# Optimization experiments

Hardware: AMD Instinct MI355X
Metric: run time of the kernel (lower is better)

The kernel has to match this reference:

```python
import jax, jax.numpy as jnp
import numpy as np

B, T = 64, 1024
VOCAB, EMBED, HIDDEN = 55, 64, 128


def setup_inputs() -> dict:
    key = jax.random.key(0)
    ks = jax.random.split(key, 15)
    stdv = 1.0 / np.sqrt(HIDDEN)
    u = lambda k, s: jax.random.uniform(k, s, jnp.float32, -stdv, stdv)
    return {
        "x": jax.random.randint(ks[0], (B, T), 0, VOCAB),
        "emb": jax.random.normal(ks[1], (VOCAB, EMBED), jnp.float32),
        "w_ih0": u(ks[2], (HIDDEN, EMBED)),
        "b_ih0": u(ks[3], (HIDDEN,)),
        "w_hh0": u(ks[4], (HIDDEN, HIDDEN)),
        "b_hh0": u(ks[5], (HIDDEN,)),
        "w_ih1": u(ks[6], (HIDDEN, HIDDEN)),
        "b_ih1": u(ks[7], (HIDDEN,)),
        "w_hh1": u(ks[8], (HIDDEN, HIDDEN)),
        "b_hh1": u(ks[9], (HIDDEN,)),
        "attn_w": u(ks[10], (HIDDEN, HIDDEN)),
        "attn_b": u(ks[11], (HIDDEN,)),
        "fc_w": u(ks[12], (VOCAB, 2 * HIDDEN)),
        "fc_b": u(ks[13], (VOCAB,)),
    }


def reference(x, emb, w_ih0, b_ih0, w_hh0, b_hh0, w_ih1, b_ih1, w_hh1, b_hh1,
              attn_w, attn_b, fc_w, fc_b):
    Bx, Tx = x.shape
    H = w_hh0.shape[0]
    e = emb[x]  # [B, T, E]

    def step(carry, x_t):  # x_t: [B, E]
        h0, h1 = carry
        h0 = jnp.tanh(x_t @ w_ih0.T + b_ih0 + h0 @ w_hh0.T + b_hh0)
        h1 = jnp.tanh(h0 @ w_ih1.T + b_ih1 + h1 @ w_hh1.T + b_hh1)
        return (h0, h1), h1

    init = (jnp.zeros((Bx, H), e.dtype), jnp.zeros((Bx, H), e.dtype))
    _, outs = jax.lax.scan(step, init, jnp.swapaxes(e, 0, 1))  # [T, B, H]
    outs = jnp.swapaxes(outs, 0, 1)  # [B, T, H]

    Q = outs @ attn_w.T + attn_b  # [B, T, H]
    scores = jnp.einsum('bth,bsh->bts', Q, outs) / jnp.sqrt(jnp.asarray(H, e.dtype))
    causal = jnp.tril(jnp.ones((Tx, Tx), bool))  # [T, T]
    scores = jnp.where(causal[None], scores, jnp.asarray(-jnp.inf, scores.dtype))
    attn = jax.nn.softmax(scores, axis=-1)
    context = jnp.einsum('bts,bsh->bth', attn, outs)  # [B, T, H]

    combined = jnp.concatenate([outs, context], axis=-1)  # [B, T, 2H]
    logits = combined @ fc_w.T + fc_b  # [B, T, vocab]
    return logits
```

## Files before the change

kernel.cpp:

```cpp
#include <hip/hip_runtime.h>
#include <hip/hip_bf16.h>
#include <cstdint>
#include <cstddef>


typedef __attribute__((ext_vector_type(8))) short short8;
typedef __attribute__((ext_vector_type(4))) float f32x4;

__device__ __forceinline__ float bf2f(unsigned short u) {
    union { unsigned int i; float f; } c; c.i = ((unsigned int)u) << 16; return c.f;
}
__device__ __forceinline__ unsigned short f2bf(float f) {
    union { float f; unsigned int i; } c; c.f = f;
    unsigned int u = c.i;
    u += 0x7fffu + ((u >> 16) & 1u);
    return (unsigned short)(u >> 16);
}
__device__ __forceinline__ unsigned int pk_bf16(float lo, float hi) {
    union { __hip_bfloat162 h2; unsigned int u; } c;
    c.h2 = __float22bfloat162_rn(make_float2(lo, hi));
    return c.u;
}
__device__ __forceinline__ float fast_tanh(float x) {
    float e = __expf(2.0f * x);
    return 1.0f - 2.0f * __builtin_amdgcn_rcpf(e + 1.0f);
}
__device__ __forceinline__ void bar_lds() {
    asm volatile("s_waitcnt lgkmcnt(0)\n\ts_barrier" ::: "memory");
}
__device__ __forceinline__ short8 ld_a_bf16(const float* p) {
    const float4* q = (const float4*)p;
    float4 f0 = q[0], f1 = q[1];
    short8 r;
    r[0]=(short)f2bf(f0.x); r[1]=(short)f2bf(f0.y);
    r[2]=(short)f2bf(f0.z); r[3]=(short)f2bf(f0.w);
    r[4]=(short)f2bf(f1.x); r[5]=(short)f2bf(f1.y);
    r[6]=(short)f2bf(f1.z); r[7]=(short)f2bf(f1.w);
    return r;
}
__device__ __forceinline__ void ld_fc_hilo(const float* p, short8& hi, short8& lo) {
    const float4* q = (const float4*)p;
    float4 f0 = q[0], f1 = q[1];
    float ff[8] = {f0.x, f0.y, f0.z, f0.w, f1.x, f1.y, f1.z, f1.w};
#pragma unroll
    for (int i = 0; i < 8; ++i) {
        unsigned short hb = f2bf(ff[i]);
        hi[i] = (short)hb;
        lo[i] = (short)f2bf(ff[i] - bf2f(hb));
    }
}

__global__ __launch_bounds__(128)
void k_we(const float* __restrict__ emb, const float* __restrict__ w_ih0,
          const float* __restrict__ b_ih0, const float* __restrict__ b_hh0,
          float* __restrict__ WE)
{
    __shared__ float ev[64];
    const int i = threadIdx.x;
    const int v = blockIdx.x;
    if (i < 64) ev[i] = emb[v * 64 + i];
    __syncthreads();
    float s = b_ih0[i] + b_hh0[i];
    const float* wr = w_ih0 + i * 64;
#pragma unroll
    for (int k = 0; k < 64; ++k) s += wr[k] * ev[k];
    WE[v * 128 + i] = s;
}

__global__ __launch_bounds__(256)
void k_weg(const int* __restrict__ x, const float* __restrict__ WE,
           float* __restrict__ WEg)
{
    __shared__ int xv[32];
    const int tid = threadIdx.x;
    const int b   = blockIdx.y;
    const int t0  = blockIdx.x * 32;
    if (tid < 32) xv[tid] = x[b * 1024 + t0 + tid];
    __syncthreads();
#pragma unroll
    for (int it = 0; it < 4; ++it) {
        int tt = it * 8 + (tid >> 5);
        int c4 = tid & 31;
        float4 v = ((const float4*)(WE + xv[tt] * 128))[c4];
        ((float4*)(WEg + ((size_t)b * 1024 + t0 + tt) * 128))[c4] = v;
    }
}

__global__ __launch_bounds__(512, 1)
void k_scan5(const float* __restrict__ WEg,
             const float* __restrict__ w_hh0,
             const float* __restrict__ w_ih1, const float* __restrict__ b_ih1,
             const float* __restrict__ w_hh1, const float* __restrict__ b_hh1,
             unsigned short* __restrict__ outs_bf)
{
    const int tid   = threadIdx.x;
    const int w     = tid >> 6;
    const int lane  = tid & 63;
    const int quad  = lane >> 4;
    const int n     = lane & 15;
    const int bbase = blockIdx.x * 16;

    __shared__ __align__(16) unsigned short h0buf[2][16][136];
    __shared__ __align__(16) unsigned short h1buf[2][16][136];

    if (w < 4) {
        const int r0 = w * 32 + quad * 4;
        const int r1 = r0 + 16;
        short8 a0[2][4];
#pragma unroll
        for (int r = 0; r < 2; ++r) {
            const size_t mrow = (size_t)(w * 32 + r * 16 + n) * 128;
#pragma unroll
            for (int ks = 0; ks < 4; ++ks)
                a0[r][ks] = ld_a_bf16(w_hh0 + mrow + ks * 32 + quad * 8);
        }
        const size_t wegB0 = (size_t)(bbase + n) * 131072 + r0;
        const size_t wegB1 = wegB0 + 16;
        {
            float4 p0 = *(const float4*)(WEg + wegB0);
            float4 p1 = *(const float4*)(WEg + wegB1);
            *(uint2*)&h0buf[0][n][r0] = make_uint2(
                pk_bf16(fast_tanh(p0.x), fast_tanh(p0.y)),
                pk_bf16(fast_tanh(p0.z), fast_tanh(p0.w)));
            *(uint2*)&h0buf[0][n][r1] = make_uint2(
                pk_bf16(fast_tanh(p1.x), fast_tanh(p1.y)),
                pk_bf16(fast_tanh(p1.z), fast_tanh(p1.w)));
        }
        float4 wA0 = *(const float4*)(WEg + wegB0 + 128);
        float4 wA1 = *(const float4*)(WEg + wegB1 + 128);
        float4 wB0 = *(const float4*)(WEg + wegB0 + 256);
        float4 wB1 = *(const float4*)(WEg + wegB1 + 256);
        float4 wC0 = *(const float4*)(WEg + wegB0 + 384);
        float4 wC1 = *(const float4*)(WEg + wegB1 + 384);
        __syncthreads();

        for (int t = 0; t < 1024; ++t) {
            const int p = t & 1;
            if (t < 1023) {
                const unsigned short* h0p = &h0buf[p][n][quad * 8];
                short8 bh[4];
#pragma unroll
                for (int ks = 0; ks < 4; ++ks)
                    bh[ks] = *(const short8*)(h0p + ks * 32);
                f32x4 c0 = (f32x4){wA0.x, wA0.y, wA0.z, wA0.w};
                f32x4 c1 = (f32x4){wA1.x, wA1.y, wA1.z, wA1.w};
#pragma unroll
                for (int ks = 0; ks < 4; ++ks) {
                    c0 = __builtin_amdgcn_mfma_f32_16x16x32_bf16(a0[0][ks], bh[ks], c0, 0,0,0);
                    c1 = __builtin_amdgcn_mfma_f32_16x16x32_bf16(a0[1][ks], bh[ks], c1, 0,0,0);
                }
                wA0 = wB0; wA1 = wB1; wB0 = wC0; wB1 = wC1;
                const size_t tpre = (size_t)((t + 4 < 1024) ? t + 4 : 1023) * 128;
                wC0 = *(const float4*)(WEg + wegB0 + tpre);
                wC1 = *(const float4*)(WEg + wegB1 + tpre);
                *(uint2*)&h0buf[p ^ 1][n][r0] = make_uint2(
                    pk_bf16(fast_tanh(c0[0]), fast_tanh(c0[1])),
                    pk_bf16(fast_tanh(c0[2]), fast_tanh(c0[3])));
                *(uint2*)&h0buf[p ^ 1][n][r1] = make_uint2(
                    pk_bf16(fast_tanh(c1[0]), fast_tanh(c1[1])),
                    pk_bf16(fast_tanh(c1[2]), fast_tanh(c1[3])));
            }
            bar_lds();
        }
    } else {
        const int w2 = w - 4;
        const int r0 = w2 * 32 + quad * 4;
        const int r1 = r0 + 16;
        short8 a1[2][4], a2[2][4];
#pragma unroll
        for (int r = 0; r < 2; ++r) {
            const size_t mrow = (size_t)(w2 * 32 + r * 16 + n) * 128;
#pragma unroll
            for (int ks = 0; ks < 4; ++ks) {
                a1[r][ks] = ld_a_bf16(w_ih1 + mrow + ks * 32 + quad * 8);
                a2[r][ks] = ld_a_bf16(w_hh1 + mrow + ks * 32 + quad * 8);
            }
        }
        f32x4 b1i[2];
#pragma unroll
        for (int r = 0; r < 2; ++r)
#pragma unroll
            for (int j = 0; j < 4; ++j) {
                int row = w2 * 32 + r * 16 + quad * 4 + j;
                b1i[r][j] = b_ih1[row] + b_hh1[row];
            }
        *(uint2*)&h1buf[0][n][r0] = make_uint2(0u, 0u);
        *(uint2*)&h1buf[0][n][r1] = make_uint2(0u, 0u);
        unsigned short* outp0 = outs_bf + (size_t)(bbase + n) * 131072 + r0;
        unsigned short* outp1 = outp0 + 16;
        __syncthreads();

        for (int t = 0; t < 1024; ++t) {
            const int p = t & 1;
            const unsigned short* h0p = &h0buf[p][n][quad * 8];
            const unsigned short* h1p = &h1buf[p][n][quad * 8];
            short8 bh0[4], bh1[4];
#pragma unroll
            for (int ks = 0; ks < 4; ++ks) {
                bh0[ks] = *(const short8*)(h0p + ks * 32);
                bh1[ks] = *(const short8*)(h1p + ks * 32);
            }
            f32x4 c0 = b1i[0], c1 = b1i[1];
            f32x4 d0 = (f32x4){0.f,0.f,0.f,0.f}, d1 = (f32x4){0.f,0.f,0.f,0.f};
#pragma unroll
            for (int ks = 0; ks < 4; ++ks) {
                c0 = __builtin_amdgcn_mfma_f32_16x16x32_bf16(a1[0][ks], bh0[ks], c0, 0,0,0);
                c1 = __builtin_amdgcn_mfma_f32_16x16x32_bf16(a1[1][ks], bh0[ks], c1, 0,0,0);
                d0 = __builtin_amdgcn_mfma_f32_16x16x32_bf16(a2[0][ks], bh1[ks], d0, 0,0,0);
                d1 = __builtin_amdgcn_mfma_f32_16x16x32_bf16(a2[1][ks], bh1[ks], d1, 0,0,0);
            }
            uint2 o0 = make_uint2(
                pk_bf16(fast_tanh(c0[0] + d0[0]), fast_tanh(c0[1] + d0[1])),
                pk_bf16(fast_tanh(c0[2] + d0[2]), fast_tanh(c0[3] + d0[3])));
            uint2 o1 = make_uint2(
                pk_bf16(fast_tanh(c1[0] + d1[0]), fast_tanh(c1[1] + d1[1])),
                pk_bf16(fast_tanh(c1[2] + d1[2]), fast_tanh(c1[3] + d1[3])));
            *(uint2*)&h1buf[p ^ 1][n][r0] = o0;
            *(uint2*)&h1buf[p ^ 1][n][r1] = o1;
            *(uint2*)(outp0 + (size_t)t * 128) = o0;
            *(uint2*)(outp1 + (size_t)t * 128) = o1;
            bar_lds();
        }
    }
}

__global__ __launch_bounds__(256)
void k_transpose(const unsigned short* __restrict__ outs_bf,
                 unsigned short* __restrict__ outsT)
{
    __shared__ unsigned short lt[128][130];
    const int tid = threadIdx.x;
    const int t0  = blockIdx.x * 128;
    const int b   = blockIdx.y;
    const unsigned int* src =
        (const unsigned int*)(outs_bf + ((size_t)b * 1024 + t0) * 128);
    for (int idx = tid; idx < 8192; idx += 256) {
        int tr = idx >> 6, h2 = idx & 63;
        unsigned int v = src[tr * 64 + h2];
        lt[tr][h2 * 2]     = (unsigned short)(v & 0xffffu);
        lt[tr][h2 * 2 + 1] = (unsigned short)(v >> 16);
    }
    __syncthreads();
    unsigned int* dst = (unsigned int*)(outsT + (size_t)b * 128 * 1024);
    for (int idx = tid; idx < 8192; idx += 256) {
        int h = idx >> 6, t2 = idx & 63;
        unsigned int v = (unsigned int)lt[t2 * 2][h] |
                         ((unsigned int)lt[t2 * 2 + 1][h] << 16);
        dst[h * 512 + (t0 >> 1) + t2] = v;
    }
}

__global__ __launch_bounds__(512, 1)
void k_attnfc(const unsigned short* __restrict__ outs_bf,
              const unsigned short* __restrict__ outsT,
              const float* __restrict__ attn_w, const float* __restrict__ attn_b,
              const float* __restrict__ fc_w, const float* __restrict__ fc_b,
              float* __restrict__ out)
{
    __shared__ __align__(16) unsigned char smem[100352];
    unsigned short* lK = (unsigned short*)smem;
    unsigned short* lV = (unsigned short*)(smem + 32768);
    unsigned short* lP = (unsigned short*)(smem + 65536);

    const int tid  = threadIdx.x;
    const int w    = tid >> 6;
    const int lane = tid & 63;
    const int quad = lane >> 4;
    const int n    = lane & 15;
    const int qt   = blockIdx.x;
    const int b    = blockIdx.y;
    unsigned short* lPw = lP + w * 2176;
    const float cscale = 0.08838834764831845f;

    const unsigned short* outsB = outs_bf + (size_t)b * 131072;
    const int qrow = qt * 128 + w * 16 + n;

    short8 bo[4];
#pragma unroll
    for (int ks = 0; ks < 4; ++ks)
        bo[ks] = *(const short8*)(outsB + (size_t)qrow * 128 + ks * 32 + quad * 8);
#pragma unroll
    for (int mt = 0; mt < 8; ++mt) {
        short8 aw[4];
#pragma unroll
        for (int ks = 0; ks < 4; ++ks)
            aw[ks] = ld_a_bf16(attn_w + (size_t)(mt * 16 + n) * 128 + ks * 32 + quad * 8);
        f32x4 cq;
#pragma unroll
        for (int r = 0; r < 4; ++r) cq[r] = attn_b[mt * 16 + quad * 4 + r];
#pragma unroll
        for (int ks = 0; ks < 4; ++ks)
            cq = __builtin_amdgcn_mfma_f32_16x16x32_bf16(aw[ks], bo[ks], cq, 0,0,0);
        *(uint2*)&lPw[n * 136 + mt * 16 + quad * 4] =
            make_uint2(pk_bf16(cq[0], cq[1]), pk_bf16(cq[2], cq[3]));
    }
    short8 qf[4];
#pragma unroll
    for (int ks = 0; ks < 4; ++ks)
        qf[ks] = *(const short8*)&lPw[n * 136 + ks * 32 + quad * 8];

    f32x4 accO[8];
#pragma unroll
    for (int dt = 0; dt < 8; ++dt) accO[dt] = (f32x4){0.f, 0.f, 0.f, 0.f};
    float mx = -1e30f, lsum = 0.f;

    for (int kt = 0; kt <= qt; ++kt) {
        __syncthreads();
        for (int c = tid; c < 2048; c += 512) {
            int row = c >> 4, k8 = c & 15;
            uint4 vk = *(const uint4*)(outsB + (size_t)(kt * 128 + row) * 128 + k8 * 8);
            *(uint4*)&lK[row * 128 + ((k8 ^ (row & 15)) << 3)] = vk;
            uint4 vv = *(const uint4*)(outsT + ((size_t)b * 128 + row) * 1024 +
                                       kt * 128 + k8 * 8);
            *(uint4*)&lV[row * 128 + ((k8 ^ (row & 15)) << 3)] = vv;
        }
        __syncthreads();
        f32x4 accS[8];
#pragma unroll
        for (int mt = 0; mt < 8; ++mt) {
            short8 af[4];
#pragma unroll
            for (int ks = 0; ks < 4; ++ks) {
                int r = mt * 16 + n;
                af[ks] = *(const short8*)&lK[r * 128 + (((ks * 4 + quad) ^ (r & 15)) << 3)];
            }
            f32x4 s = (f32x4){0.f, 0.f, 0.f, 0.f};
#pragma unroll
            for (int ks = 0; ks < 4; ++ks)
                s = __builtin_amdgcn_mfma_f32_16x16x32_bf16(af[ks], qf[ks], s, 0,0,0);
            accS[mt] = s;
        }
        if (kt == qt) {
            const int ql = w * 16 + n;
#pragma unroll
            for (int mt = 0; mt < 8; ++mt)
#pragma unroll
                for (int jv = 0; jv < 4; ++jv)
                    if (mt * 16 + quad * 4 + jv > ql) accS[mt][jv] = -1e30f;
        }
        float tmax = accS[0][0];
#pragma unroll
        for (int mt = 0; mt < 8; ++mt)
#pragma unroll
            for (int jv = 0; jv < 4; ++jv) tmax = fmaxf(tmax, accS[mt][jv]);
        tmax = fmaxf(tmax, __shfl_xor(tmax, 16));
        tmax = fmaxf(tmax, __shfl_xor(tmax, 32));
        float nm = fmaxf(mx, tmax);
        float alpha = __expf((mx - nm) * cscale);
        float ss = 0.f;
#pragma unroll
        for (int mt = 0; mt < 8; ++mt)
#pragma unroll
            for (int jv = 0; jv < 4; ++jv) {
                float p = __expf((accS[mt][jv] - nm) * cscale);
                accS[mt][jv] = p;
                ss += p;
            }
        ss += __shfl_xor(ss, 16);
        ss += __shfl_xor(ss, 32);
        lsum = lsum * alpha + ss;
        mx = nm;
#pragma unroll
        for (int mt = 0; mt < 8; ++mt)
            *(uint2*)&lPw[n * 136 + mt * 16 + quad * 4] = make_uint2(
                pk_bf16(accS[mt][0], accS[mt][1]),
                pk_bf16(accS[mt][2], accS[mt][3]));
#pragma unroll
        for (int dt = 0; dt < 8; ++dt)
#pragma unroll
            for (int jv = 0; jv < 4; ++jv) accO[dt][jv] *= alpha;
        short8 pf[4];
#pragma unroll
        for (int ks = 0; ks < 4; ++ks)
            pf[ks] = *(const short8*)&lPw[n * 136 + ks * 32 + quad * 8];
#pragma unroll
        for (int dt = 0; dt < 8; ++dt) {
            short8 vf[4];
#pragma unroll
            for (int ks = 0; ks < 4; ++ks) {
                int d = dt * 16 + n;
                vf[ks] = *(const short8*)&lV[d * 128 + (((ks * 4 + quad) ^ (d & 15)) << 3)];
            }
#pragma unroll
            for (int ks = 0; ks < 4; ++ks)
                accO[dt] = __builtin_amdgcn_mfma_f32_16x16x32_bf16(vf[ks], pf[ks], accO[dt], 0,0,0);
        }
    }
    {
        float inv = __builtin_amdgcn_rcpf(lsum);
#pragma unroll
        for (int dt = 0; dt < 8; ++dt)
            *(uint2*)&lPw[n * 136 + dt * 16 + quad * 4] = make_uint2(
                pk_bf16(accO[dt][0] * inv, accO[dt][1] * inv),
                pk_bf16(accO[dt][2] * inv, accO[dt][3] * inv));
    }
    short8 bC[4];
#pragma unroll
    for (int ks = 0; ks < 4; ++ks)
        bC[ks] = *(const short8*)&lPw[n * 136 + ks * 32 + quad * 8];
#pragma unroll
    for (int mt = 0; mt < 4; ++mt) {
        const int vrow = mt * 16 + n;
        f32x4 acc;
#pragma unroll
        for (int r = 0; r < 4; ++r) {
            int vv = mt * 16 + quad * 4 + r;
            acc[r] = (vv < 55) ? fc_b[vv] : 0.f;
        }
#pragma unroll
        for (int c = 0; c < 8; ++c) {
            short8 hi, lo;
            if (vrow < 55) {
                ld_fc_hilo(fc_w + (size_t)vrow * 256 + c * 32 + quad * 8, hi, lo);
            } else {
#pragma unroll
                for (int i = 0; i < 8; ++i) { hi[i] = 0; lo[i] = 0; }
            }
            short8 bb = (c < 4) ? bo[c] : bC[c - 4];
            acc = __builtin_amdgcn_mfma_f32_16x16x32_bf16(hi, bb, acc, 0,0,0);
            acc = __builtin_amdgcn_mfma_f32_16x16x32_bf16(lo, bb, acc, 0,0,0);
        }
#pragma unroll
        for (int r = 0; r < 4; ++r) {
            int vv = mt * 16 + quad * 4 + r;
            if (vv < 55)
                out[((size_t)b * 1024 + qrow) * 55 + vv] = acc[r];
        }
    }
}

extern "C" void kernel_launch(void* const* d_in, const int* in_sizes, int n_in,
                              void* d_out, int out_size, void* d_ws, size_t ws_size,
                              hipStream_t stream)
{
    const int*   x      = (const int*)d_in[0];
    const float* emb    = (const float*)d_in[1];
    const float* w_ih0  = (const float*)d_in[2];
    const float* b_ih0  = (const float*)d_in[3];
    const float* w_hh0  = (const float*)d_in[4];
    const float* b_hh0  = (const float*)d_in[5];
    const float* w_ih1  = (const float*)d_in[6];
    const float* b_ih1  = (const float*)d_in[7];
    const float* w_hh1  = (const float*)d_in[8];
    const float* b_hh1  = (const float*)d_in[9];
    const float* attn_w = (const float*)d_in[10];
    const float* attn_b = (const float*)d_in[11];
    const float* fc_w   = (const float*)d_in[12];
    const float* fc_b   = (const float*)d_in[13];
    float* out = (float*)d_out;

    char* ws = (char*)d_ws;
    unsigned short* outs_bf = (unsigned short*)(ws);
    unsigned short* outsT   = (unsigned short*)(ws + ((size_t)16 << 20));
    float*          WEp     = (float*)         (ws + ((size_t)32 << 20));
    float*          WEg     = (float*)         (ws + ((size_t)33 << 20));

    k_we<<<dim3(55), dim3(128), 0, stream>>>(emb, w_ih0, b_ih0, b_hh0, WEp);
    k_weg<<<dim3(32, 64), dim3(256), 0, stream>>>(x, WEp, WEg);
    k_scan5<<<dim3(4), dim3(512), 0, stream>>>(
        WEg, w_hh0, w_ih1, b_ih1, w_hh1, b_hh1, outs_bf);
    k_transpose<<<dim3(8, 64), dim3(256), 0, stream>>>(outs_bf, outsT);
    k_attnfc<<<dim3(8, 64), dim3(512), 0, stream>>>(
        outs_bf, outsT, attn_w, attn_b, fc_w, fc_b, out);
}
```

Baseline: 786.2 us.

## Merge the two RNN layer wave groups into one so each wave computes both layers

The scan kernel previously split 8 waves into a layer-0 group and a layer-1 group that exchanged hidden state through LDS, with layer 0 one step ahead. Now 4 waves each compute the layer-0 and layer-1 MFMAs for their row slice in one step. This halves the threads taking part in each per-step barrier and removes the idle branch on the last step. The loop is also unrolled by two with fixed double-buffer slots and a shorter WEg prefetch distance. In exchange, each wave holds three weight fragments in registers and runs a longer MFMA chain per step.

```diff
diff --git a/kernel.cpp b/kernel.cpp
--- a/kernel.cpp
+++ b/kernel.cpp
@@ -86,8 +86,56 @@
     }
 }
 
-__global__ __launch_bounds__(512, 1)
-void k_scan5(const float* __restrict__ WEg,
+#define SCAN_STEP(T, P, WS0, WS1)                                              \
+  {                                                                            \
+    const unsigned short* h0p = &h0buf[P][n][quad * 8];                        \
+    const unsigned short* h1p = &h1buf[P][n][quad * 8];                        \
+    short8 bh0[4], bh1[4];                                                     \
+    _Pragma("unroll")                                                          \
+    for (int ks = 0; ks < 4; ++ks) {                                           \
+      bh0[ks] = *(const short8*)(h0p + ks * 32);                               \
+      bh1[ks] = *(const short8*)(h1p + ks * 32);                               \
+    }                                                                          \
+    f32x4 c0 = (f32x4){WS0.x, WS0.y, WS0.z, WS0.w};                            \
+    f32x4 c1 = (f32x4){WS1.x, WS1.y, WS1.z, WS1.w};                            \
+    {                                                                          \
+      const size_t tpre = (size_t)(((T) + 3 < 1024) ? (T) + 3 : 1023) * 128;   \
+      WS0 = *(const float4*)(WEg + wegB0 + tpre);                              \
+      WS1 = *(const float4*)(WEg + wegB1 + tpre);                              \
+    }                                                                          \
+    f32x4 e0 = b1i[0], e1 = b1i[1];                                            \
+    f32x4 f0 = (f32x4){0.f, 0.f, 0.f, 0.f};                                    \
+    f32x4 f1 = (f32x4){0.f, 0.f, 0.f, 0.f};                                    \
+    _Pragma("unroll")                                                          \
+    for (int ks = 0; ks < 4; ++ks) {                                           \
+      c0 = __builtin_amdgcn_mfma_f32_16x16x32_bf16(a0[0][ks], bh0[ks], c0, 0, 0, 0); \
+      c1 = __builtin_amdgcn_mfma_f32_16x16x32_bf16(a0[1][ks], bh0[ks], c1, 0, 0, 0); \
+      e0 = __builtin_amdgcn_mfma_f32_16x16x32_bf16(a1[0][ks], bh0[ks], e0, 0, 0, 0); \
+      e1 = __builtin_amdgcn_mfma_f32_16x16x32_bf16(a1[1][ks], bh0[ks], e1, 0, 0, 0); \
+      f0 = __builtin_amdgcn_mfma_f32_16x16x32_bf16(a2[0][ks], bh1[ks], f0, 0, 0, 0); \
+      f1 = __builtin_amdgcn_mfma_f32_16x16x32_bf16(a2[1][ks], bh1[ks], f1, 0, 0, 0); \
+    }                                                                          \
+    *(uint2*)&h0buf[(P) ^ 1][n][r0] = make_uint2(                              \
+        pk_bf16(fast_tanh(c0[0]), fast_tanh(c0[1])),                           \
+        pk_bf16(fast_tanh(c0[2]), fast_tanh(c0[3])));                          \
+    *(uint2*)&h0buf[(P) ^ 1][n][r1] = make_uint2(                              \
+        pk_bf16(fast_tanh(c1[0]), fast_tanh(c1[1])),                           \
+        pk_bf16(fast_tanh(c1[2]), fast_tanh(c1[3])));                          \
+    uint2 o0 = make_uint2(                                                     \
+        pk_bf16(fast_tanh(e0[0] + f0[0]), fast_tanh(e0[1] + f0[1])),           \
+        pk_bf16(fast_tanh(e0[2] + f0[2]), fast_tanh(e0[3] + f0[3])));          \
+    uint2 o1 = make_uint2(                                                     \
+        pk_bf16(fast_tanh(e1[0] + f1[0]), fast_tanh(e1[1] + f1[1])),           \
+        pk_bf16(fast_tanh(e1[2] + f1[2]), fast_tanh(e1[3] + f1[3])));          \
+    *(uint2*)&h1buf[(P) ^ 1][n][r0] = o0;                                      \
+    *(uint2*)&h1buf[(P) ^ 1][n][r1] = o1;                                      \
+    *(uint2*)(outp0 + (size_t)(T) * 128) = o0;                                 \
+    *(uint2*)(outp1 + (size_t)(T) * 128) = o1;                                 \
+    bar_lds();                                                                 \
+  }
+
+__global__ __launch_bounds__(256, 1)
+void k_scan6(const float* __restrict__ WEg,
              const float* __restrict__ w_hh0,
              const float* __restrict__ w_ih1, const float* __restrict__ b_ih1,
              const float* __restrict__ w_hh1, const float* __restrict__ b_hh1,
@@ -103,124 +151,56 @@
     __shared__ __align__(16) unsigned short h0buf[2][16][136];
     __shared__ __align__(16) unsigned short h1buf[2][16][136];
 
-    if (w < 4) {
-        const int r0 = w * 32 + quad * 4;
-        const int r1 = r0 + 16;
-        short8 a0[2][4];
-#pragma unroll
-        for (int r = 0; r < 2; ++r) {
-            const size_t mrow = (size_t)(w * 32 + r * 16 + n) * 128;
-#pragma unroll
-            for (int ks = 0; ks < 4; ++ks)
-                a0[r][ks] = ld_a_bf16(w_hh0 + mrow + ks * 32 + quad * 8);
-        }
-        const size_t wegB0 = (size_t)(bbase + n) * 131072 + r0;
-        const size_t wegB1 = wegB0 + 16;
-        {
-            float4 p0 = *(const float4*)(WEg + wegB0);
-            float4 p1 = *(const float4*)(WEg + wegB1);
-            *(uint2*)&h0buf[0][n][r0] = make_uint2(
-                pk_bf16(fast_tanh(p0.x), fast_tanh(p0.y)),
-                pk_bf16(fast_tanh(p0.z), fast_tanh(p0.w)));
-            *(uint2*)&h0buf[0][n][r1] = make_uint2(
-                pk_bf16(fast_tanh(p1.x), fast_tanh(p1.y)),
-                pk_bf16(fast_tanh(p1.z), fast_tanh(p1.w)));
-        }
-        float4 wA0 = *(const float4*)(WEg + wegB0 + 128);
-        float4 wA1 = *(const float4*)(WEg + wegB1 + 128);
-        float4 wB0 = *(const float4*)(WEg + wegB0 + 256);
-        float4 wB1 = *(const float4*)(WEg + wegB1 + 256);
-        float4 wC0 = *(const float4*)(WEg + wegB0 + 384);
-        float4 wC1 = *(const float4*)(WEg + wegB1 + 384);
-        __syncthreads();
-
-        for (int t = 0; t < 1024; ++t) {
-            const int p = t & 1;
-            if (t < 1023) {
-                const unsigned short* h0p = &h0buf[p][n][quad * 8];
-                short8 bh[4];
-#pragma unroll
-                for (int ks = 0; ks < 4; ++ks)
-                    bh[ks] = *(const short8*)(h0p + ks * 32);
-                f32x4 c0 = (f32x4){wA0.x, wA0.y, wA0.z, wA0.w};
-                f32x4 c1 = (f32x4){wA1.x, wA1.y, wA1.z, wA1.w};
-#pragma unroll
-                for (int ks = 0; ks < 4; ++ks) {
-                    c0 = __builtin_amdgcn_mfma_f32_16x16x32_bf16(a0[0][ks], bh[ks], c0, 0,0,0);
-                    c1 = __builtin_amdgcn_mfma_f32_16x16x32_bf16(a0[1][ks], bh[ks], c1, 0,0,0);
-                }
-                wA0 = wB0; wA1 = wB1; wB0 = wC0; wB1 = wC1;
-                const size_t tpre = (size_t)((t + 4 < 1024) ? t + 4 : 1023) * 128;
-                wC0 = *(const float4*)(WEg + wegB0 + tpre);
-                wC1 = *(const float4*)(WEg + wegB1 + tpre);
-                *(uint2*)&h0buf[p ^ 1][n][r0] = make_uint2(
-                    pk_bf16(fast_tanh(c0[0]), fast_tanh(c0[1])),
-                    pk_bf16(fast_tanh(c0[2]), fast_tanh(c0[3])));
-                *(uint2*)&h0buf[p ^ 1][n][r1] = make_uint2(
-                    pk_bf16(fast_tanh(c1[0]), fast_tanh(c1[1])),
-                    pk_bf16(fast_tanh(c1[2]), fast_tanh(c1[3])));
-            }
-            bar_lds();
-        }
-    } else {
-        const int w2 = w - 4;
-        const int r0 = w2 * 32 + quad * 4;
-        const int r1 = r0 + 16;
-        short8 a1[2][4], a2[2][4];
-#pragma unroll
-        for (int r = 0; r < 2; ++r) {
-            const size_t mrow = (size_t)(w2 * 32 + r * 16 + n) * 128;
-#pragma unroll
-            for (int ks = 0; ks < 4; ++ks) {
-                a1[r][ks] = ld_a_bf16(w_ih1 + mrow + ks * 32 + quad * 8);
-                a2[r][ks] = ld_a_bf16(w_hh1 + mrow + ks * 32 + quad * 8);
-            }
-        }
-        f32x4 b1i[2];
-#pragma unroll
-        for (int r = 0; r < 2; ++r)
-#pragma unroll
-            for (int j = 0; j < 4; ++j) {
-                int row = w2 * 32 + r * 16 + quad * 4 + j;
-                b1i[r][j] = b_ih1[row] + b_hh1[row];
-            }
+    const int r0 = w * 32 + quad * 4;
+    const int r1 = r0 + 16;
+
+    short8 a0[2][4], a1[2][4], a2[2][4];
+#pragma unroll
+    for (int r = 0; r < 2; ++r) {
+        const size_t mrow = (size_t)(w * 32 + r * 16 + n) * 128;
+#pragma unroll
+        for (int ks = 0; ks < 4; ++ks) {
+            a0[r][ks] = ld_a_bf16(w_hh0 + mrow + ks * 32 + quad * 8);
+            a1[r][ks] = ld_a_bf16(w_ih1 + mrow + ks * 32 + quad * 8);
+            a2[r][ks] = ld_a_bf16(w_hh1 + mrow + ks * 32 + quad * 8);
+        }
+    }
+    f32x4 b1i[2];
+#pragma unroll
+    for (int r = 0; r < 2; ++r)
+#pragma unroll
+        for (int j = 0; j < 4; ++j) {
+            int row = w * 32 + r * 16 + quad * 4 + j;
+            b1i[r][j] = b_ih1[row] + b_hh1[row];
+        }
+
+    const size_t wegB0 = (size_t)(bbase + n) * 131072 + r0;
+    const size_t wegB1 = wegB0 + 16;
+
+    {
+        float4 p0 = *(const float4*)(WEg + wegB0);
+        float4 p1 = *(const float4*)(WEg + wegB1);
+        *(uint2*)&h0buf[0][n][r0] = make_uint2(
+            pk_bf16(fast_tanh(p0.x), fast_tanh(p0.y)),
+            pk_bf16(fast_tanh(p0.z), fast_tanh(p0.w)));
+        *(uint2*)&h0buf[0][n][r1] = make_uint2(
+            pk_bf16(fast_tanh(p1.x), fast_tanh(p1.y)),
+            pk_bf16(fast_tanh(p1.z), fast_tanh(p1.w)));
         *(uint2*)&h1buf[0][n][r0] = make_uint2(0u, 0u);
         *(uint2*)&h1buf[0][n][r1] = make_uint2(0u, 0u);
-        unsigned short* outp0 = outs_bf + (size_t)(bbase + n) * 131072 + r0;
-        unsigned short* outp1 = outp0 + 16;
-        __syncthreads();
-
-        for (int t = 0; t < 1024; ++t) {
-            const int p = t & 1;
-            const unsigned short* h0p = &h0buf[p][n][quad * 8];
-            const unsigned short* h1p = &h1buf[p][n][quad * 8];
-            short8 bh0[4], bh1[4];
-#pragma unroll
-            for (int ks = 0; ks < 4; ++ks) {
-                bh0[ks] = *(const short8*)(h0p + ks * 32);
-                bh1[ks] = *(const short8*)(h1p + ks * 32);
-            }
-            f32x4 c0 = b1i[0], c1 = b1i[1];
-            f32x4 d0 = (f32x4){0.f,0.f,0.f,0.f}, d1 = (f32x4){0.f,0.f,0.f,0.f};
-#pragma unroll
-            for (int ks = 0; ks < 4; ++ks) {
-                c0 = __builtin_amdgcn_mfma_f32_16x16x32_bf16(a1[0][ks], bh0[ks], c0, 0,0,0);
-                c1 = __builtin_amdgcn_mfma_f32_16x16x32_bf16(a1[1][ks], bh0[ks], c1, 0,0,0);
-                d0 = __builtin_amdgcn_mfma_f32_16x16x32_bf16(a2[0][ks], bh1[ks], d0, 0,0,0);
-                d1 = __builtin_amdgcn_mfma_f32_16x16x32_bf16(a2[1][ks], bh1[ks], d1, 0,0,0);
-            }
-            uint2 o0 = make_uint2(
-                pk_bf16(fast_tanh(c0[0] + d0[0]), fast_tanh(c0[1] + d0[1])),
-                pk_bf16(fast_tanh(c0[2] + d0[2]), fast_tanh(c0[3] + d0[3])));
-            uint2 o1 = make_uint2(
-                pk_bf16(fast_tanh(c1[0] + d1[0]), fast_tanh(c1[1] + d1[1])),
-                pk_bf16(fast_tanh(c1[2] + d1[2]), fast_tanh(c1[3] + d1[3])));
-            *(uint2*)&h1buf[p ^ 1][n][r0] = o0;
-            *(uint2*)&h1buf[p ^ 1][n][r1] = o1;
-            *(uint2*)(outp0 + (size_t)t * 128) = o0;
-            *(uint2*)(outp1 + (size_t)t * 128) = o1;
-            bar_lds();
-        }
+    }
+    float4 wA0 = *(const float4*)(WEg + wegB0 + 128);
+    float4 wA1 = *(const float4*)(WEg + wegB1 + 128);
+    float4 wB0 = *(const float4*)(WEg + wegB0 + 256);
+    float4 wB1 = *(const float4*)(WEg + wegB1 + 256);
+
+    unsigned short* outp0 = outs_bf + (size_t)(bbase + n) * 131072 + r0;
+    unsigned short* outp1 = outp0 + 16;
+    __syncthreads();
+
+    for (int t = 0; t < 1024; t += 2) {
+        SCAN_STEP(t,     0, wA0, wA1);
+        SCAN_STEP(t + 1, 1, wB0, wB1);
     }
 }
 
@@ -457,7 +437,7 @@
 
     k_we<<<dim3(55), dim3(128), 0, stream>>>(emb, w_ih0, b_ih0, b_hh0, WEp);
     k_weg<<<dim3(32, 64), dim3(256), 0, stream>>>(x, WEp, WEg);
-    k_scan5<<<dim3(4), dim3(512), 0, stream>>>(
+    k_scan6<<<dim3(4), dim3(256), 0, stream>>>(
         WEg, w_hh0, w_ih1, b_ih1, w_hh1, b_hh1, outs_bf);
     k_transpose<<<dim3(8, 64), dim3(256), 0, stream>>>(outs_bf, outsT);
     k_attnfc<<<dim3(8, 64), dim3(512), 0, stream>>>(
```

New measurement: 964.4 us. 22.7% more time.
